# Performance work log

Measured on AMD Instinct MI355X. Metric: run time of the kernel, lower is better.

Reference implementation:

```python
import jax, jax.numpy as jnp
import numpy as np

N_NODES = 50000
N_EDGES = 800000
CHANNELS = [32, 64, 128, 128, 128]


def _edge_conv(x, src, dst, w1, b1, w2, b2):
    # PyG EdgeConv (flow source_to_target): x_i = x[dst], x_j = x[src]
    x_i = x[dst]                      # [E, C_in]
    x_j = x[src]                      # [E, C_in]
    h = jnp.concatenate([x_i, x_j - x_i], axis=-1)   # [E, 2*C_in]
    h = jax.nn.relu(h @ w1 + b1) @ w2 + b2           # [E, C_out]
    out = jax.ops.segment_max(h, dst, num_segments=N_NODES)  # scatter-max aggr
    # nodes with no incoming edges -> fill with 0 (PyG zero fill)
    return jnp.where(jnp.isneginf(out), jnp.zeros_like(out), out)


def setup_inputs() -> dict:
    key = jax.random.key(0)
    ks = jax.random.split(key, 20)
    inp = {
        "x": jax.random.normal(ks[0], (N_NODES, CHANNELS[0]), dtype=jnp.float32),
        "edge_index": jax.random.randint(ks[1], (2, N_EDGES), 0, N_NODES, dtype=jnp.int64),
    }
    for i in range(4):
        cin, cout = CHANNELS[i], CHANNELS[i + 1]
        s1 = 1.0 / np.sqrt(2 * cin)
        s2 = 1.0 / np.sqrt(cout)
        inp[f"w1_{i}"] = jax.random.uniform(ks[2 + 4 * i], (2 * cin, cout), jnp.float32, -s1, s1)
        inp[f"b1_{i}"] = jax.random.uniform(ks[3 + 4 * i], (cout,), jnp.float32, -s1, s1)
        inp[f"w2_{i}"] = jax.random.uniform(ks[4 + 4 * i], (cout, cout), jnp.float32, -s2, s2)
        inp[f"b2_{i}"] = jax.random.uniform(ks[5 + 4 * i], (cout,), jnp.float32, -s2, s2)
    return inp


def reference(x, edge_index,
              w1_0, b1_0, w2_0, b2_0,
              w1_1, b1_1, w2_1, b2_1,
              w1_2, b1_2, w2_2, b2_2,
              w1_3, b1_3, w2_3, b2_3):
    src, dst = edge_index[0], edge_index[1]
    params = [(w1_0, b1_0, w2_0, b2_0), (w1_1, b1_1, w2_1, b2_1),
              (w1_2, b1_2, w2_2, b2_2), (w1_3, b1_3, w2_3, b2_3)]
    for i, (w1, b1, w2, b2) in enumerate(params):
        x = _edge_conv(x, src, dst, w1, b1, w2, b2)
        if i != 3:
            x = jax.nn.relu(x)
    return x
```

## Files before the change

### kernel.cpp

```cpp
#include <hip/hip_runtime.h>
#include <stdint.h>
#include <math.h>

#define NN 50000
#define NE 800000
#define CAP 64

typedef __attribute__((ext_vector_type(8))) __bf16 bf16x8;
typedef __attribute__((ext_vector_type(8))) unsigned short u16x8;
typedef __attribute__((ext_vector_type(16))) float f32x16;

__global__ void fill_k(const int* __restrict__ src, const int* __restrict__ dst,
                       int* __restrict__ cnt, int* __restrict__ s_src) {
    int e = blockIdx.x * 256 + threadIdx.x;
    if (e < NE) {
        int d = dst[e];
        int p = atomicAdd(&cnt[d], 1);
        s_src[(size_t)d * CAP + p] = src[e];
    }
}

__global__ void deg_order_k(const int* __restrict__ deg, int* __restrict__ order) {
    __shared__ int lbins[64];
    __shared__ int lcur[64];
    const int tid = threadIdx.x;
    if (tid < 64) lbins[tid] = 0;
    __syncthreads();
    for (int i = tid; i < NN; i += 1024) {
        int d = deg[i];
        atomicAdd(&lbins[d < 63 ? d : 63], 1);
    }
    __syncthreads();
    if (tid == 0) {
        int s = 0;
        for (int i = 0; i < 64; ++i) { lcur[i] = s; s += lbins[i]; }
    }
    __syncthreads();
    for (int i = tid; i < NN; i += 1024) {
        int d = deg[i];
        int b = d < 63 ? d : 63;
        int p = atomicAdd(&lcur[b], 1);
        order[p] = i;
    }
}

template<int COUT>
static __device__ __forceinline__ void w2body(int t, const float* __restrict__ W2,
                                              unsigned short* __restrict__ Fhi,
                                              unsigned short* __restrict__ Flo) {
    constexpr int NT = COUT / 32, KS = COUT / 16;
    if (t >= NT * KS * 64) return;
    int frag = t >> 6, lane = t & 63;
    int nt = frag % NT, ks = frag / NT;
    int col = nt * 32 + (lane & 31);
    int k0 = ks * 16 + (lane >> 5) * 8;
    size_t base = (size_t)t * 8;
    #pragma unroll
    for (int m = 0; m < 8; ++m) {
        float w = W2[(size_t)(k0 + m) * COUT + col];
        __bf16 hb = (__bf16)w;
        float hf = (float)hb;
        __bf16 lb = (__bf16)(w - hf);
        Fhi[base + m] = __builtin_bit_cast(unsigned short, hb);
        Flo[base + m] = __builtin_bit_cast(unsigned short, lb);
    }
}

template<int CIN, int COUT>
static __device__ __forceinline__ void w1body(int t, const float* __restrict__ W1,
                                              unsigned short* __restrict__ FhiU,
                                              unsigned short* __restrict__ FloU,
                                              unsigned short* __restrict__ FhiV,
                                              unsigned short* __restrict__ FloV) {
    constexpr int KS = CIN / 16, NT = COUT / 32, NFRAG = KS * NT;
    if (t >= 2 * NFRAG * 64) return;
    int type = t / (NFRAG * 64);
    int t2 = t - type * (NFRAG * 64);
    int frag = t2 >> 6, lane = t2 & 63;
    int nt = frag % NT, ks = frag / NT;
    int col = nt * 32 + (lane & 31);
    int k0 = ks * 16 + (lane >> 5) * 8;
    unsigned short* Fh = type ? FhiV : FhiU;
    unsigned short* Fl = type ? FloV : FloU;
    size_t base = (size_t)t2 * 8;
    #pragma unroll
    for (int m = 0; m < 8; ++m) {
        int k = k0 + m;
        float wb = W1[(size_t)(CIN + k) * COUT + col];
        float w = type ? wb : (W1[(size_t)k * COUT + col] - wb);
        __bf16 hb = (__bf16)w;
        float hf = (float)hb;
        __bf16 lb = (__bf16)(w - hf);
        Fh[base + m] = __builtin_bit_cast(unsigned short, hb);
        Fl[base + m] = __builtin_bit_cast(unsigned short, lb);
    }
}

struct PrepArgs {
    const float* w2[4];
    unsigned short* fh2[4];
    unsigned short* fl2[4];
    const float* w1[4];
    unsigned short* uh[4];
    unsigned short* ul[4];
    unsigned short* vh[4];
    unsigned short* vl[4];
};

__global__ void prep_all(PrepArgs a) {
    const int t = blockIdx.x * 256 + threadIdx.x;
    switch (blockIdx.y) {
        case 0: w2body<64> (t, a.w2[0], a.fh2[0], a.fl2[0]); break;
        case 1: w2body<128>(t, a.w2[1], a.fh2[1], a.fl2[1]); break;
        case 2: w2body<128>(t, a.w2[2], a.fh2[2], a.fl2[2]); break;
        case 3: w2body<128>(t, a.w2[3], a.fh2[3], a.fl2[3]); break;
        case 4: w1body<32, 64>  (t, a.w1[0], a.uh[0], a.ul[0], a.vh[0], a.vl[0]); break;
        case 5: w1body<64, 128> (t, a.w1[1], a.uh[1], a.ul[1], a.vh[1], a.vl[1]); break;
        case 6: w1body<128, 128>(t, a.w1[2], a.uh[2], a.ul[2], a.vh[2], a.vl[2]); break;
        default: w1body<128, 128>(t, a.w1[3], a.uh[3], a.ul[3], a.vh[3], a.vl[3]); break;
    }
}

template<int CIN, int COUT, bool FIRST>
__global__ void __launch_bounds__(256, 2) node_mfma(
    const float* __restrict__ xin, const float* __restrict__ agg_in,
    const float* __restrict__ b2p,
    const unsigned short* __restrict__ FhiU, const unsigned short* __restrict__ FloU,
    const unsigned short* __restrict__ FhiV, const unsigned short* __restrict__ FloV,
    const float* __restrict__ b1,
    float* __restrict__ U, float* __restrict__ Vv)
{
    constexpr int KS = CIN / 16, NT = COUT / 32, NFRAG = KS * NT;

    __shared__ __align__(16) unsigned short w1hi[NFRAG * 512];
    __shared__ __align__(16) unsigned short w1lo[NFRAG * 512];

    const int type = blockIdx.y;
    const unsigned short* Fh = type ? FhiV : FhiU;
    const unsigned short* Fl = type ? FloV : FloU;

    const int tid = threadIdx.x;
    for (int i = tid; i < NFRAG * 64; i += 256) {
        *reinterpret_cast<u16x8*>(&w1hi[i * 8]) =
            *reinterpret_cast<const u16x8*>(&Fh[(size_t)i * 8]);
        *reinterpret_cast<u16x8*>(&w1lo[i * 8]) =
            *reinterpret_cast<const u16x8*>(&Fl[(size_t)i * 8]);
    }
    __syncthreads();

    const int wave = tid >> 6, lane = tid & 63;
    const int arow = lane & 31, ah = lane >> 5;
    const int tile = blockIdx.x * 4 + wave;
    const int node = tile * 32 + arow;
    const bool vn = node < NN;
    const float vm = vn ? 1.f : 0.f;
    const float* yrow = FIRST ? &xin[(size_t)(vn ? node : 0) * CIN]
                              : &agg_in[(size_t)(vn ? node : 0) * CIN];

    f32x16 acc[NT];
    #pragma unroll
    for (int nt = 0; nt < NT; ++nt)
        #pragma unroll
        for (int r = 0; r < 16; ++r) acc[nt][r] = 0.f;

    #pragma unroll 1
    for (int ks = 0; ks < KS; ++ks) {
        const int kof = ks * 16 + ah * 8;
        const float4 y0 = *reinterpret_cast<const float4*>(yrow + kof);
        const float4 y1 = *reinterpret_cast<const float4*>(yrow + kof + 4);

        float s0, s1, s2, s3, s4, s5, s6, s7;
        if (FIRST) {
            s0 = vm * y0.x; s1 = vm * y0.y; s2 = vm * y0.z; s3 = vm * y0.w;
            s4 = vm * y1.x; s5 = vm * y1.y; s6 = vm * y1.z; s7 = vm * y1.w;
        } else {
            const float4 b20 = *reinterpret_cast<const float4*>(b2p + kof);
            const float4 b21 = *reinterpret_cast<const float4*>(b2p + kof + 4);
            s0 = vm * fmaxf(y0.x + b20.x, 0.f);
            s1 = vm * fmaxf(y0.y + b20.y, 0.f);
            s2 = vm * fmaxf(y0.z + b20.z, 0.f);
            s3 = vm * fmaxf(y0.w + b20.w, 0.f);
            s4 = vm * fmaxf(y1.x + b21.x, 0.f);
            s5 = vm * fmaxf(y1.y + b21.y, 0.f);
            s6 = vm * fmaxf(y1.z + b21.z, 0.f);
            s7 = vm * fmaxf(y1.w + b21.w, 0.f);
        }

        bf16x8 ahi, alo;
        {
            __bf16 h;
            h = (__bf16)s0; ahi[0] = h; alo[0] = (__bf16)(s0 - (float)h);
            h = (__bf16)s1; ahi[1] = h; alo[1] = (__bf16)(s1 - (float)h);
            h = (__bf16)s2; ahi[2] = h; alo[2] = (__bf16)(s2 - (float)h);
            h = (__bf16)s3; ahi[3] = h; alo[3] = (__bf16)(s3 - (float)h);
            h = (__bf16)s4; ahi[4] = h; alo[4] = (__bf16)(s4 - (float)h);
            h = (__bf16)s5; ahi[5] = h; alo[5] = (__bf16)(s5 - (float)h);
            h = (__bf16)s6; ahi[6] = h; alo[6] = (__bf16)(s6 - (float)h);
            h = (__bf16)s7; ahi[7] = h; alo[7] = (__bf16)(s7 - (float)h);
        }

        const unsigned short* hbase = &w1hi[(size_t)(ks * NT * 64 + lane) * 8];
        const unsigned short* lbase = &w1lo[(size_t)(ks * NT * 64 + lane) * 8];
        #pragma unroll
        for (int nt = 0; nt < NT; ++nt) {
            bf16x8 bhi = __builtin_bit_cast(bf16x8,
                *reinterpret_cast<const u16x8*>(hbase + (size_t)nt * 512));
            bf16x8 blo = __builtin_bit_cast(bf16x8,
                *reinterpret_cast<const u16x8*>(lbase + (size_t)nt * 512));
            acc[nt] = __builtin_amdgcn_mfma_f32_32x32x16_bf16(ahi, bhi, acc[nt], 0, 0, 0);
            acc[nt] = __builtin_amdgcn_mfma_f32_32x32x16_bf16(ahi, blo, acc[nt], 0, 0, 0);
            acc[nt] = __builtin_amdgcn_mfma_f32_32x32x16_bf16(alo, bhi, acc[nt], 0, 0, 0);
        }
    }

    float* outp = type ? Vv : U;
    #pragma unroll
    for (int nt = 0; nt < NT; ++nt) {
        const float bb = (type == 0) ? b1[nt * 32 + (lane & 31)] : 0.f;
        #pragma unroll
        for (int r = 0; r < 16; ++r) {
            const int row = (r & 3) + 8 * (r >> 2) + 4 * ah;
            const int nr = tile * 32 + row;
            if (nr < NN)
                outp[(size_t)nr * COUT + nt * 32 + (lane & 31)] = acc[nt][r] + bb;
        }
    }
}

template<int COUT>
__global__ void __launch_bounds__(512, 2) edge_node_mfma(
    const float* __restrict__ U, const float* __restrict__ Vv,
    const int* __restrict__ s_src, const int* __restrict__ deg,
    const int* __restrict__ order,
    const unsigned short* __restrict__ Fhi, const unsigned short* __restrict__ Flo,
    float* __restrict__ agg,
    const float* __restrict__ b2fin, float* __restrict__ outfin)
{
    constexpr int KS = COUT / 16;
    constexpr int NT = COUT / 32;
    constexpr int NFRAG = KS * NT;

    __shared__ __align__(16) unsigned short w2hi[NFRAG * 512];
    __shared__ __align__(16) unsigned short w2lo[NFRAG * 512];
    __shared__ __align__(16) float u_lds[16 * COUT];

    const int tid = threadIdx.x;
    for (int i = tid; i < NFRAG * 64; i += 512) {
        *reinterpret_cast<u16x8*>(&w2hi[i * 8]) =
            *reinterpret_cast<const u16x8*>(&Fhi[(size_t)i * 8]);
        *reinterpret_cast<u16x8*>(&w2lo[i * 8]) =
            *reinterpret_cast<const u16x8*>(&Flo[(size_t)i * 8]);
    }

    const int wave = tid >> 6, lane = tid & 63;
    const int arow = lane & 31;
    const int ah   = lane >> 5;
    const int isB  = arow >> 4;
    const int er   = arow & 15;

    const int pw = blockIdx.x * 8 + wave;
    const int nA = order[2 * pw];
    const int nB = order[2 * pw + 1];
    const int degA = deg[nA];
    const int degB = deg[nB];
    const int myn   = isB ? nB : nA;
    const int mydeg = isB ? degB : degA;
    const size_t myoff = (size_t)myn * CAP;

    for (int i = lane; i < COUT; i += 64) {
        u_lds[(2 * wave)     * COUT + i] = U[(size_t)nA * COUT + i];
        u_lds[(2 * wave + 1) * COUT + i] = U[(size_t)nB * COUT + i];
    }
    __syncthreads();

    const int ubase = (2 * wave + isB) * COUT;
    const int maxdeg = degA > degB ? degA : degB;

    float nmaxA[NT], nmaxB[NT];
    #pragma unroll
    for (int nt = 0; nt < NT; ++nt) { nmaxA[nt] = -INFINITY; nmaxB[nt] = -INFINITY; }

    for (int pb = 0; pb < maxdeg; pb += 16) {
        const bool valid = (pb + er) < mydeg;
        const int sv = valid ? s_src[myoff + pb + er] : 0;
        const float* vrow = &Vv[(size_t)sv * COUT];

        f32x16 acc[NT];
        #pragma unroll
        for (int nt = 0; nt < NT; ++nt)
            #pragma unroll
            for (int r = 0; r < 16; ++r) acc[nt][r] = 0.f;

        float4 vaC = *reinterpret_cast<const float4*>(vrow + ah * 8);
        float4 vbC = *reinterpret_cast<const float4*>(vrow + ah * 8 + 4);

        #pragma unroll 1
        for (int ks = 0; ks < KS; ++ks) {
            float4 vaN, vbN;
            if (ks + 1 < KS) {
                const float* vp = vrow + (ks + 1) * 16 + ah * 8;
                vaN = *reinterpret_cast<const float4*>(vp);
                vbN = *reinterpret_cast<const float4*>(vp + 4);
            }

            const int kof = ks * 16 + ah * 8;
            const float4 ua4 = *reinterpret_cast<const float4*>(&u_lds[ubase + kof]);
            const float4 ub4 = *reinterpret_cast<const float4*>(&u_lds[ubase + kof + 4]);

            bf16x8 ahi, alo;
            {
                float s; __bf16 h;
                s = fmaxf(ua4.x + vaC.x, 0.f); h = (__bf16)s; ahi[0] = h; alo[0] = (__bf16)(s - (float)h);
                s = fmaxf(ua4.y + vaC.y, 0.f); h = (__bf16)s; ahi[1] = h; alo[1] = (__bf16)(s - (float)h);
                s = fmaxf(ua4.z + vaC.z, 0.f); h = (__bf16)s; ahi[2] = h; alo[2] = (__bf16)(s - (float)h);
                s = fmaxf(ua4.w + vaC.w, 0.f); h = (__bf16)s; ahi[3] = h; alo[3] = (__bf16)(s - (float)h);
                s = fmaxf(ub4.x + vbC.x, 0.f); h = (__bf16)s; ahi[4] = h; alo[4] = (__bf16)(s - (float)h);
                s = fmaxf(ub4.y + vbC.y, 0.f); h = (__bf16)s; ahi[5] = h; alo[5] = (__bf16)(s - (float)h);
                s = fmaxf(ub4.z + vbC.z, 0.f); h = (__bf16)s; ahi[6] = h; alo[6] = (__bf16)(s - (float)h);
                s = fmaxf(ub4.w + vbC.w, 0.f); h = (__bf16)s; ahi[7] = h; alo[7] = (__bf16)(s - (float)h);
            }

            const unsigned short* hbase = &w2hi[(size_t)(ks * NT * 64 + lane) * 8];
            const unsigned short* lbase = &w2lo[(size_t)(ks * NT * 64 + lane) * 8];
            #pragma unroll
            for (int nt = 0; nt < NT; ++nt) {
                bf16x8 bhi = __builtin_bit_cast(bf16x8,
                    *reinterpret_cast<const u16x8*>(hbase + (size_t)nt * 512));
                bf16x8 blo = __builtin_bit_cast(bf16x8,
                    *reinterpret_cast<const u16x8*>(lbase + (size_t)nt * 512));
                acc[nt] = __builtin_amdgcn_mfma_f32_32x32x16_bf16(ahi, bhi, acc[nt], 0, 0, 0);
                acc[nt] = __builtin_amdgcn_mfma_f32_32x32x16_bf16(ahi, blo, acc[nt], 0, 0, 0);
                acc[nt] = __builtin_amdgcn_mfma_f32_32x32x16_bf16(alo, bhi, acc[nt], 0, 0, 0);
            }
            vaC = vaN; vbC = vbN;
        }

        #pragma unroll
        for (int nt = 0; nt < NT; ++nt) {
            float mA = -INFINITY, mB = -INFINITY;
            #pragma unroll
            for (int r = 0; r < 8; ++r) {
                const int rowA = (r & 3) + 8 * (r >> 2) + 4 * ah;
                if (pb + rowA < degA) mA = fmaxf(mA, acc[nt][r]);
            }
            #pragma unroll
            for (int r = 8; r < 16; ++r) {
                const int rowB = (r & 3) + 8 * (r >> 2) + 4 * ah - 16;
                if (pb + rowB < degB) mB = fmaxf(mB, acc[nt][r]);
            }
            mA = fmaxf(mA, __shfl_xor(mA, 32, 64));
            mB = fmaxf(mB, __shfl_xor(mB, 32, 64));
            nmaxA[nt] = fmaxf(nmaxA[nt], mA);
            nmaxB[nt] = fmaxf(nmaxB[nt], mB);
        }
    }

    if (lane < 32) {
        if (b2fin) {
            #pragma unroll
            for (int nt = 0; nt < NT; ++nt) {
                const float bb = b2fin[nt * 32 + lane];
                outfin[(size_t)nA * COUT + nt * 32 + lane] = (degA > 0) ? nmaxA[nt] + bb : 0.f;
                outfin[(size_t)nB * COUT + nt * 32 + lane] = (degB > 0) ? nmaxB[nt] + bb : 0.f;
            }
        } else {
            #pragma unroll
            for (int nt = 0; nt < NT; ++nt) {
                agg[(size_t)nA * COUT + nt * 32 + lane] = nmaxA[nt];
                agg[(size_t)nB * COUT + nt * 32 + lane] = nmaxB[nt];
            }
        }
    }
}

extern "C" void kernel_launch(void* const* d_in, const int* in_sizes, int n_in,
                              void* d_out, int out_size, void* d_ws, size_t ws_size,
                              hipStream_t stream)
{
    const float* x  = (const float*)d_in[0];
    const int*   ei = (const int*)d_in[1];
    const int* src = ei;
    const int* dst = ei + NE;

    const float *W1[4], *B1[4], *W2[4], *B2[4];
    for (int i = 0; i < 4; ++i) {
        W1[i] = (const float*)d_in[2 + 4 * i];
        B1[i] = (const float*)d_in[3 + 4 * i];
        W2[i] = (const float*)d_in[4 + 4 * i];
        B2[i] = (const float*)d_in[5 + 4 * i];
    }

    float* U   = (float*)d_ws;
    float* V   = U   + (size_t)NN * 128;
    float* agg = V   + (size_t)NN * 128;
    int* cnt     = (int*)(agg + (size_t)NN * 128);
    int* order   = cnt + NN;
    int* s_src   = order + NN;
    unsigned short* fbase = (unsigned short*)(s_src + (size_t)NN * CAP);
    unsigned short *FH2[4], *FL2[4];
    for (int i = 0; i < 4; ++i) {
        FH2[i] = fbase + (size_t)i * 32768;
        FL2[i] = FH2[i] + 16384;
    }
    unsigned short* f1base = fbase + 4 * 32768;
    unsigned short *UH[4], *UL[4], *VH[4], *VL[4];
    for (int i = 0; i < 4; ++i) {
        UH[i] = f1base + (size_t)i * 65536;
        UL[i] = UH[i] + 16384;
        VH[i] = UL[i] + 16384;
        VL[i] = VH[i] + 16384;
    }

    float* out = (float*)d_out;

    (void)hipMemsetAsync(cnt, 0, (size_t)NN * sizeof(int), stream);
    hipLaunchKernelGGL(fill_k, dim3((NE + 255) / 256), dim3(256), 0, stream,
                       src, dst, cnt, s_src);
    hipLaunchKernelGGL(deg_order_k, dim3(1), dim3(1024), 0, stream, cnt, order);

    PrepArgs pa;
    for (int i = 0; i < 4; ++i) {
        pa.w2[i] = W2[i]; pa.fh2[i] = FH2[i]; pa.fl2[i] = FL2[i];
        pa.w1[i] = W1[i]; pa.uh[i] = UH[i]; pa.ul[i] = UL[i];
        pa.vh[i] = VH[i]; pa.vl[i] = VL[i];
    }
    hipLaunchKernelGGL(prep_all, dim3(16, 8), dim3(256), 0, stream, pa);

    const int ntiles = (NN + 31) / 32;
    const dim3 gN((ntiles + 3) / 4, 2);
    const int nblkE = NN / 16;

    hipLaunchKernelGGL((node_mfma<32, 64, true>), gN, dim3(256), 0, stream,
                       x, nullptr, nullptr, UH[0], UL[0], VH[0], VL[0], B1[0], U, V);
    hipLaunchKernelGGL((edge_node_mfma<64>), dim3(nblkE), dim3(512), 0, stream,
                       U, V, s_src, cnt, order, FH2[0], FL2[0], agg,
                       (const float*)nullptr, (float*)nullptr);

    hipLaunchKernelGGL((node_mfma<64, 128, false>), gN, dim3(256), 0, stream,
                       nullptr, agg, B2[0], UH[1], UL[1], VH[1], VL[1], B1[1], U, V);
    hipLaunchKernelGGL((edge_node_mfma<128>), dim3(nblkE), dim3(512), 0, stream,
                       U, V, s_src, cnt, order, FH2[1], FL2[1], agg,
                       (const float*)nullptr, (float*)nullptr);

    hipLaunchKernelGGL((node_mfma<128, 128, false>), gN, dim3(256), 0, stream,
                       nullptr, agg, B2[1], UH[2], UL[2], VH[2], VL[2], B1[2], U, V);
    hipLaunchKernelGGL((edge_node_mfma<128>), dim3(nblkE), dim3(512), 0, stream,
                       U, V, s_src, cnt, order, FH2[2], FL2[2], agg,
                       (const float*)nullptr, (float*)nullptr);

    hipLaunchKernelGGL((node_mfma<128, 128, false>), gN, dim3(256), 0, stream,
                       nullptr, agg, B2[2], UH[3], UL[3], VH[3], VL[3], B1[3], U, V);
    hipLaunchKernelGGL((edge_node_mfma<128>), dim3(nblkE), dim3(512), 0, stream,
                       U, V, s_src, cnt, order, FH2[3], FL2[3], agg,
                       B2[3], out);
}
```

Before: 633.6 us.

## Split edge kernel output columns across grid.y and store neighbor ids as uint16

For the 128-channel layers, the edge-conv MLP kernel now splits its output column tiles over two blocks in grid.y. This halves the per-block LDS weight footprint and the accumulator registers, which should allow more occupancy. The cost is that each block recomputes the first-stage activation and gathers V rows twice. Neighbor source indices are also stored as 16-bit to halve index traffic. Node ids up to 50000 fit in unsigned short, so that part is safe.

```diff
diff --git a/kernel.cpp b/kernel.cpp
--- a/kernel.cpp
+++ b/kernel.cpp
@@ -11,12 +11,12 @@
 typedef __attribute__((ext_vector_type(16))) float f32x16;
 
 __global__ void fill_k(const int* __restrict__ src, const int* __restrict__ dst,
-                       int* __restrict__ cnt, int* __restrict__ s_src) {
+                       int* __restrict__ cnt, unsigned short* __restrict__ s_src) {
     int e = blockIdx.x * 256 + threadIdx.x;
     if (e < NE) {
         int d = dst[e];
         int p = atomicAdd(&cnt[d], 1);
-        s_src[(size_t)d * CAP + p] = src[e];
+        s_src[(size_t)d * CAP + p] = (unsigned short)src[e];
     }
 }
 
@@ -227,10 +227,10 @@
     }
 }
 
-template<int COUT>
+template<int COUT, int NTT>
 __global__ void __launch_bounds__(512, 2) edge_node_mfma(
     const float* __restrict__ U, const float* __restrict__ Vv,
-    const int* __restrict__ s_src, const int* __restrict__ deg,
+    const unsigned short* __restrict__ s_src, const int* __restrict__ deg,
     const int* __restrict__ order,
     const unsigned short* __restrict__ Fhi, const unsigned short* __restrict__ Flo,
     float* __restrict__ agg,
@@ -238,18 +238,24 @@
 {
     constexpr int KS = COUT / 16;
     constexpr int NT = COUT / 32;
-    constexpr int NFRAG = KS * NT;
-
-    __shared__ __align__(16) unsigned short w2hi[NFRAG * 512];
-    __shared__ __align__(16) unsigned short w2lo[NFRAG * 512];
+    constexpr int NFH = KS * NTT;
+
+    __shared__ __align__(16) unsigned short w2hi[NFH * 512];
+    __shared__ __align__(16) unsigned short w2lo[NFH * 512];
     __shared__ __align__(16) float u_lds[16 * COUT];
 
+    const int h = blockIdx.y;
+    const int nt0 = h * NTT;
+
     const int tid = threadIdx.x;
-    for (int i = tid; i < NFRAG * 64; i += 512) {
-        *reinterpret_cast<u16x8*>(&w2hi[i * 8]) =
-            *reinterpret_cast<const u16x8*>(&Fhi[(size_t)i * 8]);
-        *reinterpret_cast<u16x8*>(&w2lo[i * 8]) =
-            *reinterpret_cast<const u16x8*>(&Flo[(size_t)i * 8]);
+    for (int i = tid; i < NFH * 64; i += 512) {
+        const int lf = i >> 6, ln = i & 63;
+        const int ks = lf / NTT, j = lf - ks * NTT;
+        const size_t g = ((size_t)(ks * NT + nt0 + j) * 64 + ln) * 8;
+        *reinterpret_cast<u16x8*>(&w2hi[(size_t)i * 8]) =
+            *reinterpret_cast<const u16x8*>(&Fhi[g]);
+        *reinterpret_cast<u16x8*>(&w2lo[(size_t)i * 8]) =
+            *reinterpret_cast<const u16x8*>(&Flo[g]);
     }
 
     const int wave = tid >> 6, lane = tid & 63;
@@ -276,18 +282,18 @@
     const int ubase = (2 * wave + isB) * COUT;
     const int maxdeg = degA > degB ? degA : degB;
 
-    float nmaxA[NT], nmaxB[NT];
+    float nmaxA[NTT], nmaxB[NTT];
     #pragma unroll
-    for (int nt = 0; nt < NT; ++nt) { nmaxA[nt] = -INFINITY; nmaxB[nt] = -INFINITY; }
+    for (int nt = 0; nt < NTT; ++nt) { nmaxA[nt] = -INFINITY; nmaxB[nt] = -INFINITY; }
 
     for (int pb = 0; pb < maxdeg; pb += 16) {
         const bool valid = (pb + er) < mydeg;
-        const int sv = valid ? s_src[myoff + pb + er] : 0;
+        const int sv = valid ? (int)s_src[myoff + pb + er] : 0;
         const float* vrow = &Vv[(size_t)sv * COUT];
 
-        f32x16 acc[NT];
+        f32x16 acc[NTT];
         #pragma unroll
-        for (int nt = 0; nt < NT; ++nt)
+        for (int nt = 0; nt < NTT; ++nt)
             #pragma unroll
             for (int r = 0; r < 16; ++r) acc[nt][r] = 0.f;
 
@@ -309,21 +315,21 @@
 
             bf16x8 ahi, alo;
             {
-                float s; __bf16 h;
-                s = fmaxf(ua4.x + vaC.x, 0.f); h = (__bf16)s; ahi[0] = h; alo[0] = (__bf16)(s - (float)h);
-                s = fmaxf(ua4.y + vaC.y, 0.f); h = (__bf16)s; ahi[1] = h; alo[1] = (__bf16)(s - (float)h);
-                s = fmaxf(ua4.z + vaC.z, 0.f); h = (__bf16)s; ahi[2] = h; alo[2] = (__bf16)(s - (float)h);
-                s = fmaxf(ua4.w + vaC.w, 0.f); h = (__bf16)s; ahi[3] = h; alo[3] = (__bf16)(s - (float)h);
-                s = fmaxf(ub4.x + vbC.x, 0.f); h = (__bf16)s; ahi[4] = h; alo[4] = (__bf16)(s - (float)h);
-                s = fmaxf(ub4.y + vbC.y, 0.f); h = (__bf16)s; ahi[5] = h; alo[5] = (__bf16)(s - (float)h);
-                s = fmaxf(ub4.z + vbC.z, 0.f); h = (__bf16)s; ahi[6] = h; alo[6] = (__bf16)(s - (float)h);
-                s = fmaxf(ub4.w + vbC.w, 0.f); h = (__bf16)s; ahi[7] = h; alo[7] = (__bf16)(s - (float)h);
-            }
-
-            const unsigned short* hbase = &w2hi[(size_t)(ks * NT * 64 + lane) * 8];
-            const unsigned short* lbase = &w2lo[(size_t)(ks * NT * 64 + lane) * 8];
-            #pragma unroll
-            for (int nt = 0; nt < NT; ++nt) {
+                float s; __bf16 hh;
+                s = fmaxf(ua4.x + vaC.x, 0.f); hh = (__bf16)s; ahi[0] = hh; alo[0] = (__bf16)(s - (float)hh);
+                s = fmaxf(ua4.y + vaC.y, 0.f); hh = (__bf16)s; ahi[1] = hh; alo[1] = (__bf16)(s - (float)hh);
+                s = fmaxf(ua4.z + vaC.z, 0.f); hh = (__bf16)s; ahi[2] = hh; alo[2] = (__bf16)(s - (float)hh);
+                s = fmaxf(ua4.w + vaC.w, 0.f); hh = (__bf16)s; ahi[3] = hh; alo[3] = (__bf16)(s - (float)hh);
+                s = fmaxf(ub4.x + vbC.x, 0.f); hh = (__bf16)s; ahi[4] = hh; alo[4] = (__bf16)(s - (float)hh);
+                s = fmaxf(ub4.y + vbC.y, 0.f); hh = (__bf16)s; ahi[5] = hh; alo[5] = (__bf16)(s - (float)hh);
+                s = fmaxf(ub4.z + vbC.z, 0.f); hh = (__bf16)s; ahi[6] = hh; alo[6] = (__bf16)(s - (float)hh);
+                s = fmaxf(ub4.w + vbC.w, 0.f); hh = (__bf16)s; ahi[7] = hh; alo[7] = (__bf16)(s - (float)hh);
+            }
+
+            const unsigned short* hbase = &w2hi[(size_t)(ks * NTT * 64 + lane) * 8];
+            const unsigned short* lbase = &w2lo[(size_t)(ks * NTT * 64 + lane) * 8];
+            #pragma unroll
+            for (int nt = 0; nt < NTT; ++nt) {
                 bf16x8 bhi = __builtin_bit_cast(bf16x8,
                     *reinterpret_cast<const u16x8*>(hbase + (size_t)nt * 512));
                 bf16x8 blo = __builtin_bit_cast(bf16x8,
@@ -336,7 +342,7 @@
         }
 
         #pragma unroll
-        for (int nt = 0; nt < NT; ++nt) {
+        for (int nt = 0; nt < NTT; ++nt) {
             float mA = -INFINITY, mB = -INFINITY;
             #pragma unroll
             for (int r = 0; r < 8; ++r) {
@@ -358,16 +364,18 @@
     if (lane < 32) {
         if (b2fin) {
             #pragma unroll
-            for (int nt = 0; nt < NT; ++nt) {
-                const float bb = b2fin[nt * 32 + lane];
-                outfin[(size_t)nA * COUT + nt * 32 + lane] = (degA > 0) ? nmaxA[nt] + bb : 0.f;
-                outfin[(size_t)nB * COUT + nt * 32 + lane] = (degB > 0) ? nmaxB[nt] + bb : 0.f;
+            for (int nt = 0; nt < NTT; ++nt) {
+                const int col = (nt0 + nt) * 32 + lane;
+                const float bb = b2fin[col];
+                outfin[(size_t)nA * COUT + col] = (degA > 0) ? nmaxA[nt] + bb : 0.f;
+                outfin[(size_t)nB * COUT + col] = (degB > 0) ? nmaxB[nt] + bb : 0.f;
             }
         } else {
             #pragma unroll
-            for (int nt = 0; nt < NT; ++nt) {
-                agg[(size_t)nA * COUT + nt * 32 + lane] = nmaxA[nt];
-                agg[(size_t)nB * COUT + nt * 32 + lane] = nmaxB[nt];
+            for (int nt = 0; nt < NTT; ++nt) {
+                const int col = (nt0 + nt) * 32 + lane;
+                agg[(size_t)nA * COUT + col] = nmaxA[nt];
+                agg[(size_t)nB * COUT + col] = nmaxB[nt];
             }
         }
     }
@@ -395,8 +403,8 @@
     float* agg = V   + (size_t)NN * 128;
     int* cnt     = (int*)(agg + (size_t)NN * 128);
     int* order   = cnt + NN;
-    int* s_src   = order + NN;
-    unsigned short* fbase = (unsigned short*)(s_src + (size_t)NN * CAP);
+    unsigned short* s_src = (unsigned short*)(order + NN);
+    unsigned short* fbase = s_src + (size_t)NN * CAP;
     unsigned short *FH2[4], *FL2[4];
     for (int i = 0; i < 4; ++i) {
         FH2[i] = fbase + (size_t)i * 32768;
@@ -432,25 +440,25 @@
 
     hipLaunchKernelGGL((node_mfma<32, 64, true>), gN, dim3(256), 0, stream,
                        x, nullptr, nullptr, UH[0], UL[0], VH[0], VL[0], B1[0], U, V);
-    hipLaunchKernelGGL((edge_node_mfma<64>), dim3(nblkE), dim3(512), 0, stream,
+    hipLaunchKernelGGL((edge_node_mfma<64, 2>), dim3(nblkE, 1), dim3(512), 0, stream,
                        U, V, s_src, cnt, order, FH2[0], FL2[0], agg,
                        (const float*)nullptr, (float*)nullptr);
 
     hipLaunchKernelGGL((node_mfma<64, 128, false>), gN, dim3(256), 0, stream,
                        nullptr, agg, B2[0], UH[1], UL[1], VH[1], VL[1], B1[1], U, V);
-    hipLaunchKernelGGL((edge_node_mfma<128>), dim3(nblkE), dim3(512), 0, stream,
+    hipLaunchKernelGGL((edge_node_mfma<128, 2>), dim3(nblkE, 2), dim3(512), 0, stream,
                        U, V, s_src, cnt, order, FH2[1], FL2[1], agg,
                        (const float*)nullptr, (float*)nullptr);
 
     hipLaunchKernelGGL((node_mfma<128, 128, false>), gN, dim3(256), 0, stream,
                        nullptr, agg, B2[1], UH[2], UL[2], VH[2], VL[2], B1[2], U, V);
-    hipLaunchKernelGGL((edge_node_mfma<128>), dim3(nblkE), dim3(512), 0, stream,
+    hipLaunchKernelGGL((edge_node_mfma<128, 2>), dim3(nblkE, 2), dim3(512), 0, stream,
                        U, V, s_src, cnt, order, FH2[2], FL2[2], agg,
                        (const float*)nullptr, (float*)nullptr);
 
     hipLaunchKernelGGL((node_mfma<128, 128, false>), gN, dim3(256), 0, stream,
                        nullptr, agg, B2[2], UH[3], UL[3], VH[3], VL[3], B1[3], U, V);
-    hipLaunchKernelGGL((edge_node_mfma<128>), dim3(nblkE), dim3(512), 0, stream,
+    hipLaunchKernelGGL((edge_node_mfma<128, 2>), dim3(nblkE, 2), dim3(512), 0, stream,
                        U, V, s_src, cnt, order, FH2[3], FL2[3], agg,
                        B2[3], out);
 }
```

New measurement: 758.5 us. +19.7%, slower.
